# Optimization experiments

Measured on AMD Instinct MI355X. Metric: run time of the kernel, lower is better.

The kernel has to match this reference:

```python
import jax, jax.numpy as jnp
import numpy as np
import math

N, T, D, H = 64, 256, 768, 256

def setup_inputs() -> dict:
    key = jax.random.key(0)
    ks = jax.random.split(key, 5)
    s = 0.02
    return {
        "x": jax.random.normal(ks[0], (N, T, D), dtype=jnp.float32),
        "Wq": jax.random.normal(ks[1], (H, D), dtype=jnp.float32) * s,
        "Wk": jax.random.normal(ks[2], (H, D), dtype=jnp.float32) * s,
        "Wv": jax.random.normal(ks[3], (H, D), dtype=jnp.float32) * s,
        "Wo": jax.random.normal(ks[4], (D, H), dtype=jnp.float32) * s,
    }

def reference(x, Wq, Wk, Wv, Wo):
    # flatten [N,T,D] -> [M,D], full self-attention over all M tokens
    n, t, d = x.shape
    xf = x.reshape(n * t, d)                      # [M, D]
    q = xf @ Wq.T                                  # [M, H]
    k = xf @ Wk.T                                  # [M, H]
    v = xf @ Wv.T                                  # [M, H]
    scale = 1.0 / math.sqrt(q.shape[-1])
    att = jax.nn.softmax((q @ k.T) * scale, axis=-1)  # [M, M]
    pooled = (att @ v) @ Wo.T                      # [M, D]
    return pooled.mean(axis=0, keepdims=True)      # [1, D]
```

## Files before the change

### kernel.cpp

```cpp
#include <hip/hip_runtime.h>


typedef unsigned short u16;
typedef __attribute__((ext_vector_type(8))) unsigned short u16x8;
typedef __bf16 bf16x8 __attribute__((ext_vector_type(8)));
typedef float f32x4 __attribute__((ext_vector_type(4)));

#define AS1 __attribute__((address_space(1)))
#define AS3 __attribute__((address_space(3)))

#define MTOK 16384
#define DDIM 768
#define HDIM 256
#define SM_SCALE 0.0625f

#define OFF_XB    (size_t)0
#define OFF_WCAT  (size_t)25165824
#define OFF_QB    (size_t)26345472
#define OFF_KB    (size_t)34734080
#define OFF_VF    (size_t)43122688
#define OFF_RS    (size_t)59899904
#define OFF_RINV  (size_t)59965440
#define OFF_CA    (size_t)60030976
#define OFF_P     (size_t)60096512
#define WS_NEED   (size_t)60097536

__device__ __forceinline__ u16 f2bf(float f) {
  union { float f; unsigned u; } v; v.f = f;
  unsigned r = v.u + 0x7fffu + ((v.u >> 16) & 1u);
  return (u16)(r >> 16);
}

__global__ void k_conv(const float* __restrict__ src, u16* __restrict__ dst, int n8) {
  int i = blockIdx.x * blockDim.x + threadIdx.x;
  if (i >= n8) return;
  const float4* s = (const float4*)src;
  float4 a = s[2 * i], b = s[2 * i + 1];
  u16x8 o = { f2bf(a.x), f2bf(a.y), f2bf(a.z), f2bf(a.w),
              f2bf(b.x), f2bf(b.y), f2bf(b.z), f2bf(b.w) };
  *(u16x8*)(dst + (size_t)i * 8) = o;
}

__device__ __forceinline__ void stage_tile(const u16* __restrict__ g, int ld,
                                           u16* lds, int wid, int lane) {
  const int r = lane >> 2;
  const int c = (lane & 3) * 8;
#pragma unroll
  for (int i = 0; i < 2; ++i) {
    int ii = wid * 2 + i;
    const u16* gp = g + (size_t)(ii * 16 + r) * ld + c;
    __builtin_amdgcn_global_load_lds((const AS1 unsigned int*)gp,
                                     (AS3 unsigned int*)(lds + ii * 512), 16, 0, 0);
  }
}

#define KSTEP(APTR, LDA, BPTR, LDB)                                           \
  {                                                                           \
    stage_tile((APTR), (LDA), As, wid, lane);                                 \
    stage_tile((BPTR), (LDB), Bs, wid, lane);                                 \
    __syncthreads();                                                          \
    bf16x8 af[4], bfr[4];                                                     \
    const int kk = (lane >> 4) * 8;                                           \
    _Pragma("unroll") for (int m = 0; m < 4; ++m)                             \
        af[m] = *(const bf16x8*)(As + (wm * 64 + m * 16 + (lane & 15)) * 32 + kk); \
    _Pragma("unroll") for (int n = 0; n < 4; ++n)                             \
        bfr[n] = *(const bf16x8*)(Bs + (wn * 64 + n * 16 + (lane & 15)) * 32 + kk); \
    _Pragma("unroll") for (int m = 0; m < 4; ++m)                             \
        _Pragma("unroll") for (int n = 0; n < 4; ++n)                         \
            acc[m][n] = __builtin_amdgcn_mfma_f32_16x16x32_bf16(              \
                af[m], bfr[n], acc[m][n], 0, 0, 0);                           \
    __syncthreads();                                                          \
  }

__global__ __launch_bounds__(256, 2) void k_qkv(const u16* __restrict__ Xb,
                                                const u16* __restrict__ Wcat,
                                                u16* __restrict__ Qb,
                                                u16* __restrict__ Kb,
                                                float* __restrict__ Vf) {
  __shared__ u16 As[128 * 32];
  __shared__ u16 Bs[128 * 32];
  const int tid = threadIdx.x, wid = tid >> 6, lane = tid & 63;
  const int wm = wid >> 1, wn = wid & 1;
  const int row0 = blockIdx.x * 128;
  const int col0 = blockIdx.y * 128;
  f32x4 acc[4][4] = {};
  for (int k0 = 0; k0 < DDIM; k0 += 32) {
    KSTEP(Xb + (size_t)row0 * DDIM + k0, DDIM,
          Wcat + (size_t)col0 * DDIM + k0, DDIM);
  }
#pragma unroll
  for (int m = 0; m < 4; ++m)
#pragma unroll
    for (int n = 0; n < 4; ++n) {
      int col = col0 + wn * 64 + n * 16 + (lane & 15);
#pragma unroll
      for (int j = 0; j < 4; ++j) {
        int row = row0 + wm * 64 + m * 16 + (lane >> 4) * 4 + j;
        float v = acc[m][n][j];
        if (col < 256)      Qb[(size_t)row * HDIM + col]         = f2bf(v);
        else if (col < 512) Kb[(size_t)row * HDIM + (col - 256)] = f2bf(v);
        else                Vf[(size_t)row * HDIM + (col - 512)] = v;
      }
    }
}


template <int PASS>
__global__ __launch_bounds__(512, 2) void k_spass(const u16* __restrict__ Qb,
                                                  const u16* __restrict__ Kb,
                                                  const float* __restrict__ rinv,
                                                  float* __restrict__ dst) {
  __shared__ u16 sh[81920];
  const int tid = threadIdx.x, wid = tid >> 6, lane = tid & 63;
  const int wm = wid >> 2, wn = wid & 3;
  const int rp = blockIdx.x >> 3;
  const int cg = blockIdx.x & 7;

  const int l15 = lane & 15;
  const int akey = (lane & 7) << 4;
  const int bkey = ((l15 ^ (l15 >> 2)) & 3) << 4;
  const int bcol = (((lane >> 4) * 16) ^ bkey) >> 1;
  const int a_srow = lane >> 5;
  const int a_scol = (lane & 31) * 16;
  const int b_srow = lane >> 2;
  const int b_scol = ((lane & 3) * 16) ^ ((((lane >> 2) & 3) ^ ((lane >> 4) & 3)) << 4);

  f32x4 acc[8][4] = {};
  float aux[8][4];
#pragma unroll
  for (int mi = 0; mi < 8; ++mi)
#pragma unroll
    for (int j = 0; j < 4; ++j)
      aux[mi][j] = (PASS == 1) ? 0.0f
          : rinv[rp * 256 + wm * 128 + mi * 16 + (lane >> 4) * 4 + j];

  {
    const char* gA = (const char*)Qb + (size_t)(rp * 256) * 512;
#pragma unroll
    for (int j = 0; j < 16; ++j) {
      const int i = wid * 16 + j;
      const int row = i * 2 + a_srow;
      const char* src = gA + (size_t)row * 512 + (a_scol ^ ((row & 7) << 4));
      __builtin_amdgcn_global_load_lds((const AS1 unsigned int*)src,
                                       (AS3 unsigned int*)(sh + i * 512), 16, 0, 0);
    }
  }

#define STAGE_B(S)                                                            \
  {                                                                           \
    const int ct_ = cg * 8 + ((S) >> 3), t_ = (S) & 7;                        \
    const char* gB = (const char*)Kb + (size_t)(ct_ * 256) * 512 + t_ * 64;   \
    u16* dl = sh + 65536 + ((S) & 1) * 8192;                                  \
    _Pragma("unroll") for (int j = 0; j < 2; ++j) {                           \
      const int i = wid * 2 + j;                                              \
      const char* src = gB + (size_t)(i * 16 + b_srow) * 512 + b_scol;        \
      __builtin_amdgcn_global_load_lds((const AS1 unsigned int*)src,          \
                                       (AS3 unsigned int*)(dl + i * 512), 16, 0, 0); \
    }                                                                         \
  }

  STAGE_B(0);

  for (int s = 0; s < 64; ++s) {
    if (s + 1 < 64) {
      STAGE_B(s + 1);
      asm volatile("s_waitcnt vmcnt(2)" ::: "memory");
    } else {
      asm volatile("s_waitcnt vmcnt(0)" ::: "memory");
    }
    __builtin_amdgcn_s_barrier();

    const int t = s & 7;
    const u16* Bb = sh + 65536 + (s & 1) * 8192;
    const int acolt = ((t * 64 + (lane >> 4) * 16) ^ akey) >> 1;

    bf16x8 bq[4];
#pragma unroll
    for (int ni = 0; ni < 4; ++ni)
      bq[ni] = *(const bf16x8*)(Bb + (wn * 64 + ni * 16 + l15) * 32 + bcol);

    __builtin_amdgcn_s_setprio(1);
#pragma unroll
    for (int mi = 0; mi < 8; ++mi) {
      bf16x8 a0 = *(const bf16x8*)(sh + (wm * 128 + mi * 16 + l15) * 256 + acolt);
#pragma unroll
      for (int ni = 0; ni < 4; ++ni)
        acc[mi][ni] = __builtin_amdgcn_mfma_f32_16x16x32_bf16(a0, bq[ni], acc[mi][ni], 0, 0, 0);
    }
    __builtin_amdgcn_s_setprio(0);
    __builtin_amdgcn_s_barrier();

    if ((s & 7) == 7) {
      if (PASS == 1) {
#pragma unroll
        for (int mi = 0; mi < 8; ++mi)
#pragma unroll
          for (int ni = 0; ni < 4; ++ni)
#pragma unroll
            for (int j = 0; j < 4; ++j)
              aux[mi][j] += __expf(acc[mi][ni][j] * SM_SCALE);
      } else {
        const int ct = cg * 8 + (s >> 3);
        float cs[4] = {};
#pragma unroll
        for (int mi = 0; mi < 8; ++mi)
#pragma unroll
          for (int ni = 0; ni < 4; ++ni)
#pragma unroll
            for (int j = 0; j < 4; ++j)
              cs[ni] += __expf(acc[mi][ni][j] * SM_SCALE) * aux[mi][j];
#pragma unroll
        for (int ni = 0; ni < 4; ++ni) {
          float v = cs[ni];
          v += __shfl_xor(v, 16);
          v += __shfl_xor(v, 32);
          if ((lane >> 4) == 0)
            atomicAdd(&dst[ct * 256 + wn * 64 + ni * 16 + l15], v);
        }
      }
#pragma unroll
      for (int mi = 0; mi < 8; ++mi)
#pragma unroll
        for (int ni = 0; ni < 4; ++ni)
          acc[mi][ni] = (f32x4){0.f, 0.f, 0.f, 0.f};
    }
  }

  if (PASS == 1) {
#pragma unroll
    for (int mi = 0; mi < 8; ++mi)
#pragma unroll
      for (int j = 0; j < 4; ++j) {
        float v = aux[mi][j];
        v += __shfl_xor(v, 1);  v += __shfl_xor(v, 2);
        v += __shfl_xor(v, 4);  v += __shfl_xor(v, 8);
        if (l15 == 0)
          atomicAdd(&dst[rp * 256 + wm * 128 + mi * 16 + (lane >> 4) * 4 + j], v);
      }
  }
}

__global__ void k_rinv(const float* __restrict__ rowsum, float* __restrict__ rinv) {
  int i = blockIdx.x * 256 + threadIdx.x;
  if (i < MTOK) rinv[i] = 1.0f / (rowsum[i] * (float)MTOK);
}

__global__ void k_p(const float* __restrict__ colacc, const float* __restrict__ Vf,
                    float* __restrict__ p) {
  const int h = threadIdx.x;
  const int r0 = blockIdx.x * 128;
  float s = 0.f;
  for (int r = r0; r < r0 + 128; ++r)
    s += colacc[r] * Vf[(size_t)r * HDIM + h];
  atomicAdd(&p[h], s);
}

__global__ void k_out(const float* __restrict__ p, const float* __restrict__ Wo,
                      float* __restrict__ out) {
  const int d = blockIdx.x * 256 + threadIdx.x;
  if (d >= DDIM) return;
  float s = 0.f;
  for (int h = 0; h < HDIM; ++h) s += p[h] * Wo[(size_t)d * HDIM + h];
  out[d] = s;
}

extern "C" void kernel_launch(void* const* d_in, const int* in_sizes, int n_in,
                              void* d_out, int out_size, void* d_ws, size_t ws_size,
                              hipStream_t stream) {
  const float* x  = (const float*)d_in[0];
  const float* Wq = (const float*)d_in[1];
  const float* Wk = (const float*)d_in[2];
  const float* Wv = (const float*)d_in[3];
  const float* Wo = (const float*)d_in[4];
  float* out = (float*)d_out;

  char* ws = (char*)d_ws;
  u16*   Xb     = (u16*)(ws + OFF_XB);
  u16*   Wcat   = (u16*)(ws + OFF_WCAT);
  u16*   Qb     = (u16*)(ws + OFF_QB);
  u16*   Kb     = (u16*)(ws + OFF_KB);
  float* Vf     = (float*)(ws + OFF_VF);
  float* rowsum = (float*)(ws + OFF_RS);
  float* rinv   = (float*)(ws + OFF_RINV);
  float* colacc = (float*)(ws + OFF_CA);
  float* p      = (float*)(ws + OFF_P);

  k_conv<<<(MTOK * DDIM / 8 + 255) / 256, 256, 0, stream>>>(x, Xb, MTOK * DDIM / 8);
  const int w8 = HDIM * DDIM / 8;
  k_conv<<<(w8 + 255) / 256, 256, 0, stream>>>(Wq, Wcat + 0 * HDIM * DDIM, w8);
  k_conv<<<(w8 + 255) / 256, 256, 0, stream>>>(Wk, Wcat + 1 * HDIM * DDIM, w8);
  k_conv<<<(w8 + 255) / 256, 256, 0, stream>>>(Wv, Wcat + 2 * HDIM * DDIM, w8);

  hipMemsetAsync(ws + OFF_RS, 0, WS_NEED - OFF_RS, stream);

  k_qkv<<<dim3(MTOK / 128, DDIM / 128), 256, 0, stream>>>(Xb, Wcat, Qb, Kb, Vf);

  k_spass<1><<<512, 512, 0, stream>>>(Qb, Kb, nullptr, rowsum);
  k_rinv<<<MTOK / 256, 256, 0, stream>>>(rowsum, rinv);
  k_spass<2><<<512, 512, 0, stream>>>(Qb, Kb, rinv, colacc);

  k_p<<<MTOK / 128, 256, 0, stream>>>(colacc, Vf, p);
  k_out<<<(DDIM + 255) / 256, 256, 0, stream>>>(p, Wo, out);
}
```

Before: 455.7 us.

## Store bf16 score matrix in pass one and replace second QK^T pass with streaming reduction

Pass one now writes the full 16384x16384 score matrix in bf16 (512 MB) to workspace in a register-fragment layout. A new kernel streams it back, applies exp with the row normalizers and accumulates the column sums, replacing the second score GEMM. This trades recomputing QK^T for about 1 GB of HBM traffic and adds bf16 rounding of the scores before the exp. It only runs when the workspace is large enough, and the barrier in the pass-one loop moves to after the epilogue.

```diff
diff --git a/kernel.cpp b/kernel.cpp
--- a/kernel.cpp
+++ b/kernel.cpp
@@ -24,11 +24,17 @@
 #define OFF_CA    (size_t)60030976
 #define OFF_P     (size_t)60096512
 #define WS_NEED   (size_t)60097536
+#define OFF_S     WS_NEED
+#define WS_NEED_F (size_t)(WS_NEED + 536870912)
 
 __device__ __forceinline__ u16 f2bf(float f) {
   union { float f; unsigned u; } v; v.f = f;
   unsigned r = v.u + 0x7fffu + ((v.u >> 16) & 1u);
   return (u16)(r >> 16);
+}
+__device__ __forceinline__ float bf2f(u16 b) {
+  union { unsigned u; float f; } v; v.u = ((unsigned)b) << 16;
+  return v.f;
 }
 
 __global__ void k_conv(const float* __restrict__ src, u16* __restrict__ dst, int n8) {
@@ -105,11 +111,12 @@
 }
 
 
-template <int PASS>
+template <int PASS, bool STORE>
 __global__ __launch_bounds__(512, 2) void k_spass(const u16* __restrict__ Qb,
                                                   const u16* __restrict__ Kb,
                                                   const float* __restrict__ rinv,
-                                                  float* __restrict__ dst) {
+                                                  float* __restrict__ dst,
+                                                  u16* __restrict__ Sp) {
   __shared__ u16 sh[81920];
   const int tid = threadIdx.x, wid = tid >> 6, lane = tid & 63;
   const int wm = wid >> 2, wn = wid & 3;
@@ -188,19 +195,33 @@
         acc[mi][ni] = __builtin_amdgcn_mfma_f32_16x16x32_bf16(a0, bq[ni], acc[mi][ni], 0, 0, 0);
     }
     __builtin_amdgcn_s_setprio(0);
-    __builtin_amdgcn_s_barrier();
 
     if ((s & 7) == 7) {
+      const int ct = s >> 3;
       if (PASS == 1) {
 #pragma unroll
-        for (int mi = 0; mi < 8; ++mi)
+        for (int mi = 0; mi < 8; ++mi) {
+          if (STORE) {
+            const size_t bw = (size_t)blockIdx.x * 8 + wid;
+            u16x8 h0 = { f2bf(acc[mi][0][0]), f2bf(acc[mi][0][1]),
+                         f2bf(acc[mi][0][2]), f2bf(acc[mi][0][3]),
+                         f2bf(acc[mi][1][0]), f2bf(acc[mi][1][1]),
+                         f2bf(acc[mi][1][2]), f2bf(acc[mi][1][3]) };
+            u16x8 h1 = { f2bf(acc[mi][2][0]), f2bf(acc[mi][2][1]),
+                         f2bf(acc[mi][2][2]), f2bf(acc[mi][2][3]),
+                         f2bf(acc[mi][3][0]), f2bf(acc[mi][3][1]),
+                         f2bf(acc[mi][3][2]), f2bf(acc[mi][3][3]) };
+            *(u16x8*)(Sp + ((bw * 128 + (ct * 8 + mi) * 2 + 0) * 64 + lane) * 8) = h0;
+            *(u16x8*)(Sp + ((bw * 128 + (ct * 8 + mi) * 2 + 1) * 64 + lane) * 8) = h1;
+          }
 #pragma unroll
           for (int ni = 0; ni < 4; ++ni)
 #pragma unroll
             for (int j = 0; j < 4; ++j)
               aux[mi][j] += __expf(acc[mi][ni][j] * SM_SCALE);
+        }
       } else {
-        const int ct = cg * 8 + (s >> 3);
+        const int CT = cg * 8 + ct;
         float cs[4] = {};
 #pragma unroll
         for (int mi = 0; mi < 8; ++mi)
@@ -215,7 +236,7 @@
           v += __shfl_xor(v, 16);
           v += __shfl_xor(v, 32);
           if ((lane >> 4) == 0)
-            atomicAdd(&dst[ct * 256 + wn * 64 + ni * 16 + l15], v);
+            atomicAdd(&dst[CT * 256 + wn * 64 + ni * 16 + l15], v);
         }
       }
 #pragma unroll
@@ -224,6 +245,7 @@
         for (int ni = 0; ni < 4; ++ni)
           acc[mi][ni] = (f32x4){0.f, 0.f, 0.f, 0.f};
     }
+    __builtin_amdgcn_s_barrier();
   }
 
   if (PASS == 1) {
@@ -237,6 +259,49 @@
         if (l15 == 0)
           atomicAdd(&dst[rp * 256 + wm * 128 + mi * 16 + (lane >> 4) * 4 + j], v);
       }
+  }
+}
+
+__global__ __launch_bounds__(512) void k_s2r(const u16* __restrict__ Sp,
+                                             const float* __restrict__ rinv,
+                                             float* __restrict__ colacc) {
+  const int tid = threadIdx.x, wid = tid >> 6, lane = tid & 63;
+  const int wm = wid >> 2, wn = wid & 3;
+  const int rp = blockIdx.x >> 3;
+  const int cg = blockIdx.x & 7;
+  const int l15 = lane & 15;
+
+  float aux[8][4];
+#pragma unroll
+  for (int mi = 0; mi < 8; ++mi)
+#pragma unroll
+    for (int j = 0; j < 4; ++j)
+      aux[mi][j] = rinv[rp * 256 + wm * 128 + mi * 16 + (lane >> 4) * 4 + j];
+
+  const size_t bw = (size_t)blockIdx.x * 8 + wid;
+  for (int ct = 0; ct < 8; ++ct) {
+    float cs[4] = {};
+#pragma unroll
+    for (int mi = 0; mi < 8; ++mi) {
+      u16x8 h0 = *(const u16x8*)(Sp + ((bw * 128 + (ct * 8 + mi) * 2 + 0) * 64 + lane) * 8);
+      u16x8 h1 = *(const u16x8*)(Sp + ((bw * 128 + (ct * 8 + mi) * 2 + 1) * 64 + lane) * 8);
+#pragma unroll
+      for (int j = 0; j < 4; ++j) {
+        cs[0] += __expf(bf2f(h0[j])     * SM_SCALE) * aux[mi][j];
+        cs[1] += __expf(bf2f(h0[4 + j]) * SM_SCALE) * aux[mi][j];
+        cs[2] += __expf(bf2f(h1[j])     * SM_SCALE) * aux[mi][j];
+        cs[3] += __expf(bf2f(h1[4 + j]) * SM_SCALE) * aux[mi][j];
+      }
+    }
+    const int CT = cg * 8 + ct;
+#pragma unroll
+    for (int ni = 0; ni < 4; ++ni) {
+      float v = cs[ni];
+      v += __shfl_xor(v, 16);
+      v += __shfl_xor(v, 32);
+      if ((lane >> 4) == 0)
+        atomicAdd(&colacc[CT * 256 + wn * 64 + ni * 16 + l15], v);
+    }
   }
 }
 
@@ -284,6 +349,9 @@
   float* rinv   = (float*)(ws + OFF_RINV);
   float* colacc = (float*)(ws + OFF_CA);
   float* p      = (float*)(ws + OFF_P);
+  u16*   Sp     = (u16*)(ws + OFF_S);
+
+  const bool fused = (ws_size >= WS_NEED_F);
 
   k_conv<<<(MTOK * DDIM / 8 + 255) / 256, 256, 0, stream>>>(x, Xb, MTOK * DDIM / 8);
   const int w8 = HDIM * DDIM / 8;
@@ -295,9 +363,15 @@
 
   k_qkv<<<dim3(MTOK / 128, DDIM / 128), 256, 0, stream>>>(Xb, Wcat, Qb, Kb, Vf);
 
-  k_spass<1><<<512, 512, 0, stream>>>(Qb, Kb, nullptr, rowsum);
-  k_rinv<<<MTOK / 256, 256, 0, stream>>>(rowsum, rinv);
-  k_spass<2><<<512, 512, 0, stream>>>(Qb, Kb, rinv, colacc);
+  if (fused) {
+    k_spass<1, true><<<512, 512, 0, stream>>>(Qb, Kb, nullptr, rowsum, Sp);
+    k_rinv<<<MTOK / 256, 256, 0, stream>>>(rowsum, rinv);
+    k_s2r<<<512, 512, 0, stream>>>(Sp, rinv, colacc);
+  } else {
+    k_spass<1, false><<<512, 512, 0, stream>>>(Qb, Kb, nullptr, rowsum, nullptr);
+    k_rinv<<<MTOK / 256, 256, 0, stream>>>(rowsum, rinv);
+    k_spass<2, false><<<512, 512, 0, stream>>>(Qb, Kb, rinv, colacc, nullptr);
+  }
 
   k_p<<<MTOK / 128, 256, 0, stream>>>(colacc, Vf, p);
   k_out<<<(DDIM + 255) / 256, 256, 0, stream>>>(p, Wo, out);
```

After: 455.4 us. Within noise of the previous version (-0.1%).
